# Optimization experiments

Hardware: AMD Instinct MI355X
Metric: run time of the kernel (lower is better)

## Reference

```python
import jax, jax.numpy as jnp
import numpy as np

T, B, IN, H = 256, 64, 512, 1024

def setup_inputs() -> dict:
    key = jax.random.key(0)
    ks = jax.random.split(key, 8)
    s_in = 1.0 / np.sqrt(IN)
    s_h = 1.0 / np.sqrt(H)
    return {
        "inp": jax.random.normal(ks[0], (T, B, IN), jnp.float32),
        "img": jax.random.normal(ks[1], (B, H), jnp.float32),
        "Wxh": jax.random.uniform(ks[2], (4 * H, IN), jnp.float32, -s_in, s_in),
        "bxh": jax.random.uniform(ks[3], (4 * H,), jnp.float32, -s_in, s_in),
        "Whh": jax.random.uniform(ks[4], (4 * H, H), jnp.float32, -s_h, s_h),
        "bhh": jax.random.uniform(ks[5], (4 * H,), jnp.float32, -s_h, s_h),
        "Wout": jax.random.uniform(ks[6], (IN, H), jnp.float32, -s_h, s_h),
        "bout": jax.random.uniform(ks[7], (IN,), jnp.float32, -s_h, s_h),
    }

def reference(inp, img, Wxh, bxh, Whh, bhh, Wout, bout):
    t_len, b, _ = inp.shape
    h_dim = Whh.shape[1]
    img4 = jnp.concatenate([img, img, img, img], axis=1)  # [B, 4H]
    # precompute input projection for all timesteps: [T, B, 4H]
    xproj = jnp.einsum('tbi,gi->tbg', inp, Wxh) + bxh
    xproj = xproj.at[0].add(img4)

    def step(carry, xg):
        h, c = carry
        gates = xg + h @ Whh.T + bhh  # [B, 4H]
        i_g, f_g, g_g, o_g = jnp.split(gates, 4, axis=1)
        c = jax.nn.sigmoid(f_g) * c + jax.nn.sigmoid(i_g) * jnp.tanh(g_g)
        h = jax.nn.sigmoid(o_g) * jnp.tanh(c)
        return (h, c), h

    zeros = jnp.zeros((b, h_dim), inp.dtype)
    _, hs = jax.lax.scan(step, (zeros, zeros), xproj)  # hs: [T, B, H]
    out = jnp.einsum('tbh,vh->tbv', hs, Wout) + bout  # [T, B, IN]
    return jax.nn.log_softmax(out, axis=-1)
```

## Files before the change

### kernel.cpp

```cpp
#include <hip/hip_runtime.h>
#include <math.h>

#define T_LEN 256
#define B_SZ  64
#define IN_D  512
#define H_D   1024
#define G4    4096

typedef float  f32x4 __attribute__((ext_vector_type(4)));
typedef short  s16x8 __attribute__((ext_vector_type(8)));
typedef unsigned short u16;
typedef unsigned int   u32;

__device__ __forceinline__ void gl_lds16(const void* g, void* l) {
  __builtin_amdgcn_global_load_lds(
      (const __attribute__((address_space(1))) unsigned int*)g,
      (__attribute__((address_space(3))) unsigned int*)l, 16, 0, 0);
}

__device__ __forceinline__ u16 f2bf(float f) {
  union { float f; unsigned u; } v; v.f = f;
  unsigned x = v.u;
  unsigned r = (x + 0x7fffu + ((x >> 16) & 1u)) >> 16;
  return (u16)r;
}
__device__ __forceinline__ float bf2f(u16 b) {
  union { unsigned u; float f; } v; v.u = ((unsigned)b) << 16;
  return v.f;
}
__device__ __forceinline__ float sigm(float x) {
  return 1.0f / (1.0f + __expf(-x));
}

__global__ void cvt_f32_bf16(const float* __restrict__ src, u16* __restrict__ dst, int n) {
  int i = blockIdx.x * blockDim.x + threadIdx.x;
  int stride = gridDim.x * blockDim.x;
  for (; i < n; i += stride) dst[i] = f2bf(src[i]);
}

template<int KD, int EPI>
__launch_bounds__(256)
__global__ void gemm_bt(const u16* __restrict__ A, const u16* __restrict__ Bm,
                        const float* __restrict__ bias, const float* __restrict__ img,
                        u16* __restrict__ Cb, float* __restrict__ Cf, int Ncols) {
  __shared__ u16 sA[128 * 64];
  __shared__ u16 sB[128 * 64];
  const int tid  = threadIdx.x;
  const int wave = tid >> 6, lane = tid & 63;
  const int wm = wave >> 1, wn = wave & 1;
  const int mBase = blockIdx.y * 128;
  const int nBase = blockIdx.x * 128;

  f32x4 acc[4][4] = {};

  for (int k0 = 0; k0 < KD; k0 += 64) {
#pragma unroll
    for (int it = 0; it < 4; ++it) {
      int s = it * 256 + tid;
      int row = s >> 3, c = s & 7;
      int gc = c ^ (row & 7);
      const u16* ga = A  + (size_t)(mBase + row) * KD + k0 + gc * 8;
      const u16* gb = Bm + (size_t)(nBase + row) * KD + k0 + gc * 8;
      gl_lds16(ga, &sA[(it * 256 + wave * 64) * 8]);
      gl_lds16(gb, &sB[(it * 256 + wave * 64) * 8]);
    }
    __syncthreads();

    const int q = lane >> 4, rl = lane & 15;
#pragma unroll
    for (int ks = 0; ks < 64; ks += 32) {
      s16x8 af[4], bfr[4];
      int gcb = (ks >> 3) + q;
#pragma unroll
      for (int i = 0; i < 4; ++i) {
        int rowA = wm * 64 + i * 16 + rl;
        af[i]  = *(const s16x8*)&sA[rowA * 64 + (gcb ^ (rowA & 7)) * 8];
        int rowB = wn * 64 + i * 16 + rl;
        bfr[i] = *(const s16x8*)&sB[rowB * 64 + (gcb ^ (rowB & 7)) * 8];
      }
#pragma unroll
      for (int i = 0; i < 4; ++i)
#pragma unroll
        for (int j = 0; j < 4; ++j)
          acc[i][j] = __builtin_amdgcn_mfma_f32_16x16x32_bf16(af[i], bfr[j], acc[i][j], 0, 0, 0);
    }
    __syncthreads();
  }

#pragma unroll
  for (int i = 0; i < 4; ++i) {
    int rbase = mBase + wm * 64 + i * 16 + ((lane >> 4) << 2);
#pragma unroll
    for (int j = 0; j < 4; ++j) {
      int col = nBase + wn * 64 + j * 16 + (lane & 15);
      float bc = bias[col];
#pragma unroll
      for (int r = 0; r < 4; ++r) {
        int row = rbase + r;
        float v = acc[i][j][r] + bc;
        if (EPI == 0) {
          if (row < B_SZ) v += img[row * H_D + (col & (H_D - 1))];
          Cb[(size_t)row * Ncols + col] = f2bf(v);
        } else {
          Cf[(size_t)row * Ncols + col] = v;
        }
      }
    }
  }
}

#define WPAD 1032
__launch_bounds__(256, 1)
__global__ void lstm_rec(const u16* __restrict__ WhhB, const u16* __restrict__ xproj,
                         const float* __restrict__ bhh, u32* __restrict__ hs32,
                         int* __restrict__ flags) {
  __shared__ u16  sW[64 * WPAD];
  __shared__ u16  sH[16 * 512];
  __shared__ float sG[4][16][16];

  const int tid  = threadIdx.x;
  const int wave = tid >> 6, lane = tid & 63;
  const int grp = blockIdx.x >> 6;
  const int wg  = blockIdx.x & 63;
  const int bBase = grp * 16;
  const int colBase = wg * 16;

  for (int it = 0; it < 32; ++it) {
    int s = it * 256 + tid;
    int n = s >> 7, c = s & 127;
    int grow = (n >> 4) * H_D + colBase + (n & 15);
    s16x8 v = *(const s16x8*)(WhhB + (size_t)grow * H_D + c * 8);
    *(s16x8*)&sW[n * WPAD + c * 8] = v;
  }
  __syncthreads();

  float cst = 0.f;
  const int ub = tid >> 4, uc = tid & 15;
  const int gb = bBase + ub;
  const int gcol = colBase + uc;
  const float bh_i = bhh[0 * H_D + gcol], bh_f = bhh[1 * H_D + gcol];
  const float bh_g = bhh[2 * H_D + gcol], bh_o = bhh[3 * H_D + gcol];
  const int q = lane >> 4, rl = lane & 15;

  for (int t = 0; t < T_LEN; ++t) {
    const u16* xp = xproj + ((size_t)t * B_SZ + gb) * G4;
    float gi_ = bf2f(xp[0 * H_D + gcol]) + bh_i;
    float gf_ = bf2f(xp[1 * H_D + gcol]) + bh_f;
    float gg_ = bf2f(xp[2 * H_D + gcol]) + bh_g;
    float go_ = bf2f(xp[3 * H_D + gcol]) + bh_o;

    if (t > 0) {
      if (tid < 64) {
        const int* fp = flags + (t - 1) * 256 + grp * 64 + tid;
        while (__hip_atomic_load(fp, __ATOMIC_RELAXED, __HIP_MEMORY_SCOPE_AGENT) == 0)
          __builtin_amdgcn_s_sleep(1);
      }
      __syncthreads();

      u32 v[32];
      const u32* hp = hs32 + (size_t)(t - 1) * B_SZ * 512 + (size_t)bBase * 512;
#pragma unroll
      for (int j = 0; j < 32; ++j) {
        int d = j * 256 + tid;
        v[j] = __hip_atomic_load(&hp[(d >> 9) * 512 + (d & 511)],
                                 __ATOMIC_RELAXED, __HIP_MEMORY_SCOPE_AGENT);
      }

      f32x4 acc = {0.f, 0.f, 0.f, 0.f};
#pragma unroll
      for (int half = 0; half < 2; ++half) {
        int chunk = tid >> 2;
        int off = (tid & 3) * 2;
#pragma unroll
        for (int r = 0; r < 16; ++r)
          *(u32*)&sH[r * 512 + ((chunk ^ (r & 7)) * 8 + off)] = v[2 * r + half];
        __syncthreads();
#pragma unroll
        for (int ks = 0; ks < 512; ks += 32) {
          int gc = (ks >> 3) + q;
          s16x8 afr = *(const s16x8*)&sH[rl * 512 + ((gc ^ (rl & 7)) & 63) * 8];
          s16x8 bfr = *(const s16x8*)&sW[(wave * 16 + rl) * WPAD + half * 512 + ks + q * 8];
          acc = __builtin_amdgcn_mfma_f32_16x16x32_bf16(afr, bfr, acc, 0, 0, 0);
        }
        __syncthreads();
      }
#pragma unroll
      for (int r = 0; r < 4; ++r)
        sG[wave][(lane >> 4) * 4 + r][lane & 15] = acc[r];
      __syncthreads();
      gi_ += sG[0][ub][uc]; gf_ += sG[1][ub][uc];
      gg_ += sG[2][ub][uc]; go_ += sG[3][ub][uc];
      __syncthreads();
    }

    cst = sigm(gf_) * cst + sigm(gi_) * tanhf(gg_);
    float h = sigm(go_) * tanhf(cst);
    u32 bits = f2bf(h);
    u32 partner = (u32)__shfl_xor((int)bits, 1);
    if ((tid & 1) == 0) {
      __hip_atomic_store(&hs32[((size_t)t * B_SZ + gb) * 512 + (gcol >> 1)],
                         bits | (partner << 16),
                         __ATOMIC_RELAXED, __HIP_MEMORY_SCOPE_AGENT);
    }
    __builtin_amdgcn_s_waitcnt(0);
    __syncthreads();
    if (tid == 0)
      __hip_atomic_store(&flags[t * 256 + grp * 64 + wg], 1,
                         __ATOMIC_RELAXED, __HIP_MEMORY_SCOPE_AGENT);
  }
}

__launch_bounds__(256)
__global__ void logsoftmax_rows(float* __restrict__ out) {
  __shared__ float red[8];
  float* p = out + (size_t)blockIdx.x * IN_D;
  const int tid = threadIdx.x;
  float v0 = p[tid], v1 = p[tid + 256];
  float m = fmaxf(v0, v1);
#pragma unroll
  for (int off = 32; off > 0; off >>= 1) m = fmaxf(m, __shfl_down(m, off));
  if ((tid & 63) == 0) red[tid >> 6] = m;
  __syncthreads();
  m = fmaxf(fmaxf(red[0], red[1]), fmaxf(red[2], red[3]));
  float e = __expf(v0 - m) + __expf(v1 - m);
#pragma unroll
  for (int off = 32; off > 0; off >>= 1) e += __shfl_down(e, off);
  if ((tid & 63) == 0) red[4 + (tid >> 6)] = e;
  __syncthreads();
  float ls = m + logf(red[4] + red[5] + red[6] + red[7]);
  p[tid] = v0 - ls;
  p[tid + 256] = v1 - ls;
}

extern "C" void kernel_launch(void* const* d_in, const int* in_sizes, int n_in,
                              void* d_out, int out_size, void* d_ws, size_t ws_size,
                              hipStream_t stream) {
  const float* inp  = (const float*)d_in[0];
  const float* img  = (const float*)d_in[1];
  const float* Wxh  = (const float*)d_in[2];
  const float* bxh  = (const float*)d_in[3];
  const float* Whh  = (const float*)d_in[4];
  const float* bhh  = (const float*)d_in[5];
  const float* Wout = (const float*)d_in[6];
  const float* bout = (const float*)d_in[7];
  float* out = (float*)d_out;

  char* ws = (char*)d_ws;
  u16* inpB   = (u16*)(ws);
  u16* WxhB   = (u16*)(ws + 16777216);
  u16* WhhB   = (u16*)(ws + 20971520);
  u16* WoutB  = (u16*)(ws + 29360128);
  u16* xprojB = (u16*)(ws + 30408704);
  u16* hsB    = (u16*)(ws + 164626432);
  int* flags  = (int*)(ws + 198180864);

  cvt_f32_bf16<<<2048, 256, 0, stream>>>(inp,  inpB,  T_LEN * B_SZ * IN_D);
  cvt_f32_bf16<<<2048, 256, 0, stream>>>(Wxh,  WxhB,  G4 * IN_D);
  cvt_f32_bf16<<<2048, 256, 0, stream>>>(Whh,  WhhB,  G4 * H_D);
  cvt_f32_bf16<<<2048, 256, 0, stream>>>(Wout, WoutB, IN_D * H_D);
  hipMemsetAsync(flags, 0, T_LEN * 256 * sizeof(int), stream);

  gemm_bt<IN_D, 0><<<dim3(G4 / 128, 16384 / 128), 256, 0, stream>>>(
      inpB, WxhB, bxh, img, xprojB, nullptr, G4);

  lstm_rec<<<256, 256, 0, stream>>>(WhhB, xprojB, bhh, (u32*)hsB, flags);

  gemm_bt<H_D, 1><<<dim3(IN_D / 128, 16384 / 128), 256, 0, stream>>>(
      hsB, WoutB, bout, nullptr, nullptr, out, IN_D);

  logsoftmax_rows<<<16384, 256, 0, stream>>>(out);
}
```

Before: 1.196 ms.

## Replace per-step flag sync with sentinel polling on h and keep Whh in registers

The recurrent kernel drops its separate flag array. hs is pre-filled with a 0xFFFFFFFF sentinel, and consumers spin on the h values themselves until they are no longer the sentinel, which removes the waitcnt, barrier and flag store on the producer side. The Whh slice now sits in registers (32 s16x8 per lane) instead of LDS. The MFMA chain is split across four accumulators, and sG is double-buffered to drop one barrier per step. This relies on a bf16 pair never legitimately equalling the sentinel (it would be a NaN pair), and it raises register pressure.

```diff
diff --git a/kernel.cpp b/kernel.cpp
--- a/kernel.cpp
+++ b/kernel.cpp
@@ -6,6 +6,7 @@
 #define IN_D  512
 #define H_D   1024
 #define G4    4096
+#define SENT  0xFFFFFFFFu
 
 typedef float  f32x4 __attribute__((ext_vector_type(4)));
 typedef short  s16x8 __attribute__((ext_vector_type(8)));
@@ -109,14 +110,11 @@
   }
 }
 
-#define WPAD 1032
 __launch_bounds__(256, 1)
 __global__ void lstm_rec(const u16* __restrict__ WhhB, const u16* __restrict__ xproj,
-                         const float* __restrict__ bhh, u32* __restrict__ hs32,
-                         int* __restrict__ flags) {
-  __shared__ u16  sW[64 * WPAD];
-  __shared__ u16  sH[16 * 512];
-  __shared__ float sG[4][16][16];
+                         const float* __restrict__ bhh, u32* __restrict__ hs32) {
+  __shared__ u16  sH[16 * 1024];
+  __shared__ float sG[2][4][16][16];
 
   const int tid  = threadIdx.x;
   const int wave = tid >> 6, lane = tid & 63;
@@ -124,15 +122,12 @@
   const int wg  = blockIdx.x & 63;
   const int bBase = grp * 16;
   const int colBase = wg * 16;
-
-  for (int it = 0; it < 32; ++it) {
-    int s = it * 256 + tid;
-    int n = s >> 7, c = s & 127;
-    int grow = (n >> 4) * H_D + colBase + (n & 15);
-    s16x8 v = *(const s16x8*)(WhhB + (size_t)grow * H_D + c * 8);
-    *(s16x8*)&sW[n * WPAD + c * 8] = v;
-  }
-  __syncthreads();
+  const int q = lane >> 4, rl = lane & 15;
+
+  s16x8 bf[32];
+#pragma unroll
+  for (int it = 0; it < 32; ++it)
+    bf[it] = *(const s16x8*)(WhhB + (size_t)(wave * H_D + colBase + rl) * H_D + it * 32 + q * 8);
 
   float cst = 0.f;
   const int ub = tid >> 4, uc = tid & 15;
@@ -140,7 +135,6 @@
   const int gcol = colBase + uc;
   const float bh_i = bhh[0 * H_D + gcol], bh_f = bhh[1 * H_D + gcol];
   const float bh_g = bhh[2 * H_D + gcol], bh_o = bhh[3 * H_D + gcol];
-  const int q = lane >> 4, rl = lane & 15;
 
   for (int t = 0; t < T_LEN; ++t) {
     const u16* xp = xproj + ((size_t)t * B_SZ + gb) * G4;
@@ -150,47 +144,57 @@
     float go_ = bf2f(xp[3 * H_D + gcol]) + bh_o;
 
     if (t > 0) {
-      if (tid < 64) {
-        const int* fp = flags + (t - 1) * 256 + grp * 64 + tid;
-        while (__hip_atomic_load(fp, __ATOMIC_RELAXED, __HIP_MEMORY_SCOPE_AGENT) == 0)
-          __builtin_amdgcn_s_sleep(1);
+      const u32* hp = hs32 + (size_t)(t - 1) * B_SZ * 512 + (size_t)bBase * 512;
+      u32 v[32];
+#pragma unroll
+      for (int i = 0; i < 8; ++i) {
+        int e = i * 256 + tid;
+        int base = (e >> 7) * 512 + (e & 127) * 4;
+#pragma unroll
+        for (int d = 0; d < 4; ++d)
+          v[i * 4 + d] = __hip_atomic_load(hp + base + d,
+                                           __ATOMIC_RELAXED, __HIP_MEMORY_SCOPE_AGENT);
+      }
+#pragma unroll
+      for (int i = 0; i < 8; ++i) {
+        int e = i * 256 + tid;
+        int base = (e >> 7) * 512 + (e & 127) * 4;
+#pragma unroll
+        for (int d = 0; d < 4; ++d)
+          while (v[i * 4 + d] == SENT)
+            v[i * 4 + d] = __hip_atomic_load(hp + base + d,
+                                             __ATOMIC_RELAXED, __HIP_MEMORY_SCOPE_AGENT);
+      }
+#pragma unroll
+      for (int i = 0; i < 8; ++i) {
+        int e = i * 256 + tid;
+        int row = e >> 7, c16 = e & 127;
+        u32* dst = (u32*)&sH[row * 1024 + (c16 ^ (row & 7)) * 8];
+        dst[0] = v[i * 4 + 0]; dst[1] = v[i * 4 + 1];
+        dst[2] = v[i * 4 + 2]; dst[3] = v[i * 4 + 3];
       }
       __syncthreads();
 
-      u32 v[32];
-      const u32* hp = hs32 + (size_t)(t - 1) * B_SZ * 512 + (size_t)bBase * 512;
-#pragma unroll
-      for (int j = 0; j < 32; ++j) {
-        int d = j * 256 + tid;
-        v[j] = __hip_atomic_load(&hp[(d >> 9) * 512 + (d & 511)],
-                                 __ATOMIC_RELAXED, __HIP_MEMORY_SCOPE_AGENT);
-      }
-
-      f32x4 acc = {0.f, 0.f, 0.f, 0.f};
-#pragma unroll
-      for (int half = 0; half < 2; ++half) {
-        int chunk = tid >> 2;
-        int off = (tid & 3) * 2;
-#pragma unroll
-        for (int r = 0; r < 16; ++r)
-          *(u32*)&sH[r * 512 + ((chunk ^ (r & 7)) * 8 + off)] = v[2 * r + half];
-        __syncthreads();
-#pragma unroll
-        for (int ks = 0; ks < 512; ks += 32) {
-          int gc = (ks >> 3) + q;
-          s16x8 afr = *(const s16x8*)&sH[rl * 512 + ((gc ^ (rl & 7)) & 63) * 8];
-          s16x8 bfr = *(const s16x8*)&sW[(wave * 16 + rl) * WPAD + half * 512 + ks + q * 8];
-          acc = __builtin_amdgcn_mfma_f32_16x16x32_bf16(afr, bfr, acc, 0, 0, 0);
-        }
-        __syncthreads();
-      }
+      f32x4 a0 = {}, a1 = {}, a2 = {}, a3 = {};
+#pragma unroll
+      for (int it = 0; it < 32; it += 4) {
+        s16x8 f0 = *(const s16x8*)&sH[rl * 1024 + ((((it + 0) * 4 + q)) ^ (rl & 7)) * 8];
+        s16x8 f1 = *(const s16x8*)&sH[rl * 1024 + ((((it + 1) * 4 + q)) ^ (rl & 7)) * 8];
+        s16x8 f2 = *(const s16x8*)&sH[rl * 1024 + ((((it + 2) * 4 + q)) ^ (rl & 7)) * 8];
+        s16x8 f3 = *(const s16x8*)&sH[rl * 1024 + ((((it + 3) * 4 + q)) ^ (rl & 7)) * 8];
+        a0 = __builtin_amdgcn_mfma_f32_16x16x32_bf16(f0, bf[it + 0], a0, 0, 0, 0);
+        a1 = __builtin_amdgcn_mfma_f32_16x16x32_bf16(f1, bf[it + 1], a1, 0, 0, 0);
+        a2 = __builtin_amdgcn_mfma_f32_16x16x32_bf16(f2, bf[it + 2], a2, 0, 0, 0);
+        a3 = __builtin_amdgcn_mfma_f32_16x16x32_bf16(f3, bf[it + 3], a3, 0, 0, 0);
+      }
+      f32x4 acc = (a0 + a1) + (a2 + a3);
+
 #pragma unroll
       for (int r = 0; r < 4; ++r)
-        sG[wave][(lane >> 4) * 4 + r][lane & 15] = acc[r];
+        sG[t & 1][wave][q * 4 + r][rl] = acc[r];
       __syncthreads();
-      gi_ += sG[0][ub][uc]; gf_ += sG[1][ub][uc];
-      gg_ += sG[2][ub][uc]; go_ += sG[3][ub][uc];
-      __syncthreads();
+      gi_ += sG[t & 1][0][ub][uc]; gf_ += sG[t & 1][1][ub][uc];
+      gg_ += sG[t & 1][2][ub][uc]; go_ += sG[t & 1][3][ub][uc];
     }
 
     cst = sigm(gf_) * cst + sigm(gi_) * tanhf(gg_);
@@ -202,11 +206,6 @@
                          bits | (partner << 16),
                          __ATOMIC_RELAXED, __HIP_MEMORY_SCOPE_AGENT);
     }
-    __builtin_amdgcn_s_waitcnt(0);
-    __syncthreads();
-    if (tid == 0)
-      __hip_atomic_store(&flags[t * 256 + grp * 64 + wg], 1,
-                         __ATOMIC_RELAXED, __HIP_MEMORY_SCOPE_AGENT);
   }
 }
 
@@ -252,18 +251,17 @@
   u16* WoutB  = (u16*)(ws + 29360128);
   u16* xprojB = (u16*)(ws + 30408704);
   u16* hsB    = (u16*)(ws + 164626432);
-  int* flags  = (int*)(ws + 198180864);
 
   cvt_f32_bf16<<<2048, 256, 0, stream>>>(inp,  inpB,  T_LEN * B_SZ * IN_D);
   cvt_f32_bf16<<<2048, 256, 0, stream>>>(Wxh,  WxhB,  G4 * IN_D);
   cvt_f32_bf16<<<2048, 256, 0, stream>>>(Whh,  WhhB,  G4 * H_D);
   cvt_f32_bf16<<<2048, 256, 0, stream>>>(Wout, WoutB, IN_D * H_D);
-  hipMemsetAsync(flags, 0, T_LEN * 256 * sizeof(int), stream);
+  hipMemsetAsync(hsB, 0xFF, (size_t)T_LEN * B_SZ * H_D * sizeof(u16), stream);
 
   gemm_bt<IN_D, 0><<<dim3(G4 / 128, 16384 / 128), 256, 0, stream>>>(
       inpB, WxhB, bxh, img, xprojB, nullptr, G4);
 
-  lstm_rec<<<256, 256, 0, stream>>>(WhhB, xprojB, bhh, (u32*)hsB, flags);
+  lstm_rec<<<256, 256, 0, stream>>>(WhhB, xprojB, bhh, (u32*)hsB);
 
   gemm_bt<H_D, 1><<<dim3(IN_D / 128, 16384 / 128), 256, 0, stream>>>(
       hsB, WoutB, bout, nullptr, nullptr, out, IN_D);
```

Result: slower. 2.337 ms (+95.4%).
